# Performance work log

Hardware: AMD Instinct MI355X
Metric: run time of the kernel (lower is better)

## Reference

```python
import jax, jax.numpy as jnp
import numpy as np
from jax import lax

B, T, F, Z, H = 256, 1024, 64, 32, 512


def _lstm_cell(x, h, c, W_ih, W_hh, b_ih, b_hh):
    # gates: [B, 4H], torch LSTMCell gate order i, f, g, o
    g = x @ W_ih.T + b_ih + h @ W_hh.T + b_hh
    i, f, gg, o = jnp.split(g, 4, axis=-1)
    c_new = jax.nn.sigmoid(f) * c + jax.nn.sigmoid(i) * jnp.tanh(gg)
    h_new = jax.nn.sigmoid(o) * jnp.tanh(c_new)
    return h_new, c_new


def setup_inputs() -> dict:
    key = jax.random.key(0)
    ks = jax.random.split(key, 12)
    s = 1.0 / np.sqrt(H)
    return {
        "input": jax.random.normal(ks[0], (B, T, F), dtype=jnp.float32),
        "z": jax.random.normal(ks[1], (B, Z, 1), dtype=jnp.float32),
        "h0": jnp.zeros((B, H), dtype=jnp.float32),
        "c0": jnp.zeros((B, H), dtype=jnp.float32),
        "W_ih1": jax.random.normal(ks[2], (4 * H, F + Z), dtype=jnp.float32) * s,
        "W_hh1": jax.random.normal(ks[3], (4 * H, H), dtype=jnp.float32) * s,
        "b_ih1": jax.random.normal(ks[4], (4 * H,), dtype=jnp.float32) * s,
        "b_hh1": jax.random.normal(ks[5], (4 * H,), dtype=jnp.float32) * s,
        "W_ih2": jax.random.normal(ks[6], (4 * H, H), dtype=jnp.float32) * s,
        "W_hh2": jax.random.normal(ks[7], (4 * H, H), dtype=jnp.float32) * s,
        "b_ih2": jax.random.normal(ks[8], (4 * H,), dtype=jnp.float32) * s,
        "b_hh2": jax.random.normal(ks[9], (4 * H,), dtype=jnp.float32) * s,
        "W_lin": jax.random.normal(ks[10], (1, H), dtype=jnp.float32) * s,
        "b_lin": jax.random.normal(ks[11], (1,), dtype=jnp.float32) * s,
    }


def reference(input, z, h0, c0, W_ih1, W_hh1, b_ih1, b_hh1,
              W_ih2, W_hh2, b_ih2, b_hh2, W_lin, b_lin):
    zf = z[:, :, 0]  # [B, Z], concatenated at every step
    # torch loop iterates i = T-1 ... 0; scan over time-reversed inputs
    xs = jnp.swapaxes(input, 0, 1)[::-1]  # [T, B, F]

    def step(carry, x_t):
        h1, c1, h2, c2 = carry
        xin = jnp.concatenate([x_t, zf], axis=1)  # [B, F+Z]
        h1, c1 = _lstm_cell(xin, h1, c1, W_ih1, W_hh1, b_ih1, b_hh1)
        h2, c2 = _lstm_cell(h1, h2, c2, W_ih2, W_hh2, b_ih2, b_hh2)
        return (h1, c1, h2, c2), h2

    _, ys = lax.scan(step, (h0, c0, h0, c0), xs)
    # outputs[i] = h2 at loop index i; outputs[-1] = outputs[T-1] = first scan step
    last_out = ys[0]
    return last_out @ W_lin.T + b_lin
```

## Files before the change

kernel.cpp:

```cpp
#include <hip/hip_runtime.h>
#include <math.h>

#define NB 256
#define NT 1024
#define NF 64
#define NZ 32
#define NH 512


__device__ __forceinline__ float sigmoidf_(float x) {
    return 1.0f / (1.0f + __expf(-x));
}

__global__ __launch_bounds__(256) void k_prep(
    const float* __restrict__ input, const float* __restrict__ z,
    const float* __restrict__ b_lin, float* __restrict__ xinT,
    float* __restrict__ out)
{
    int idx = blockIdx.x * 256 + threadIdx.x;
    int k  = idx >> 8;
    int bt = idx & 255;
    float v;
    if (k < NF) v = input[(size_t)bt * (NT * NF) + (size_t)(NT - 1) * NF + k];
    else        v = z[bt * NZ + (k - NF)];
    xinT[k * NB + bt] = v;
    if (idx < NB) out[idx] = b_lin[0];
}

__global__ __launch_bounds__(256) void k_lstm1(
    const float* __restrict__ W_ih1, const float* __restrict__ b_ih1,
    const float* __restrict__ b_hh1, const float* __restrict__ xinT,
    float* __restrict__ h1T)
{
    const int lane = threadIdx.x & 63;
    const int wv   = __builtin_amdgcn_readfirstlane(threadIdx.x >> 6);
    const int btb  = blockIdx.x & 3;
    const int jb   = blockIdx.x >> 2;
    const int bt   = btb * 64 + lane;
    const int j0   = jb * 16 + wv * 4;
    const int K    = NF + NZ;

    float acc[4][3];
    #pragma unroll
    for (int jj = 0; jj < 4; ++jj)
        acc[jj][0] = acc[jj][1] = acc[jj][2] = 0.0f;

    const float* __restrict__ wi[4];
    const float* __restrict__ wg[4];
    const float* __restrict__ wo[4];
    #pragma unroll
    for (int jj = 0; jj < 4; ++jj) {
        int j = j0 + jj;
        wi[jj] = W_ih1 + (size_t)j * K;
        wg[jj] = W_ih1 + (size_t)(1024 + j) * K;
        wo[jj] = W_ih1 + (size_t)(1536 + j) * K;
    }

    #pragma unroll 4
    for (int k = 0; k < K; ++k) {
        float h = xinT[k * NB + bt];
        #pragma unroll
        for (int jj = 0; jj < 4; ++jj) {
            acc[jj][0] = fmaf(wi[jj][k], h, acc[jj][0]);
            acc[jj][1] = fmaf(wg[jj][k], h, acc[jj][1]);
            acc[jj][2] = fmaf(wo[jj][k], h, acc[jj][2]);
        }
    }

    #pragma unroll
    for (int jj = 0; jj < 4; ++jj) {
        int j = j0 + jj;
        float gi = acc[jj][0] + b_ih1[j]        + b_hh1[j];
        float gg = acc[jj][1] + b_ih1[1024 + j] + b_hh1[1024 + j];
        float go = acc[jj][2] + b_ih1[1536 + j] + b_hh1[1536 + j];
        float c1 = sigmoidf_(gi) * tanhf(gg);
        float h1 = sigmoidf_(go) * tanhf(c1);
        h1T[j * NB + bt] = h1;
    }
}

__global__ __launch_bounds__(256) void k_lstm2(
    const float* __restrict__ W_ih2, const float* __restrict__ b_ih2,
    const float* __restrict__ b_hh2, const float* __restrict__ W_lin,
    const float* __restrict__ h1T, float* __restrict__ out)
{
    const int lane = threadIdx.x & 63;
    const int wv   = __builtin_amdgcn_readfirstlane(threadIdx.x >> 6);
    const int btb  = blockIdx.x & 3;
    const int jb   = blockIdx.x >> 2;
    const int bt   = btb * 64 + lane;
    const int j0   = jb * 8 + wv * 2;

    float acc[2][3];
    #pragma unroll
    for (int jj = 0; jj < 2; ++jj)
        acc[jj][0] = acc[jj][1] = acc[jj][2] = 0.0f;

    const float* __restrict__ wi[2];
    const float* __restrict__ wg[2];
    const float* __restrict__ wo[2];
    #pragma unroll
    for (int jj = 0; jj < 2; ++jj) {
        int j = j0 + jj;
        wi[jj] = W_ih2 + (size_t)j * NH;
        wg[jj] = W_ih2 + (size_t)(1024 + j) * NH;
        wo[jj] = W_ih2 + (size_t)(1536 + j) * NH;
    }

    #pragma unroll 8
    for (int k = 0; k < NH; ++k) {
        float h = h1T[k * NB + bt];
        #pragma unroll
        for (int jj = 0; jj < 2; ++jj) {
            acc[jj][0] = fmaf(wi[jj][k], h, acc[jj][0]);
            acc[jj][1] = fmaf(wg[jj][k], h, acc[jj][1]);
            acc[jj][2] = fmaf(wo[jj][k], h, acc[jj][2]);
        }
    }

    float partial = 0.0f;
    #pragma unroll
    for (int jj = 0; jj < 2; ++jj) {
        int j = j0 + jj;
        float gi = acc[jj][0] + b_ih2[j]        + b_hh2[j];
        float gg = acc[jj][1] + b_ih2[1024 + j] + b_hh2[1024 + j];
        float go = acc[jj][2] + b_ih2[1536 + j] + b_hh2[1536 + j];
        float c2 = sigmoidf_(gi) * tanhf(gg);
        float h2 = sigmoidf_(go) * tanhf(c2);
        partial  = fmaf(h2, W_lin[j], partial);
    }
    atomicAdd(out + bt, partial);
}

extern "C" void kernel_launch(void* const* d_in, const int* in_sizes, int n_in,
                              void* d_out, int out_size, void* d_ws, size_t ws_size,
                              hipStream_t stream) {
    const float* input = (const float*)d_in[0];
    const float* z     = (const float*)d_in[1];
    const float* W_ih1 = (const float*)d_in[4];
    const float* b_ih1 = (const float*)d_in[6];
    const float* b_hh1 = (const float*)d_in[7];
    const float* W_ih2 = (const float*)d_in[8];
    const float* b_ih2 = (const float*)d_in[10];
    const float* b_hh2 = (const float*)d_in[11];
    const float* W_lin = (const float*)d_in[12];
    const float* b_lin = (const float*)d_in[13];

    float* out  = (float*)d_out;
    float* xinT = (float*)d_ws;
    float* h1T  = xinT + 96 * NB;

    k_prep <<< 96, 256, 0, stream>>>(input, z, b_lin, xinT, out);
    k_lstm1<<<128, 256, 0, stream>>>(W_ih1, b_ih1, b_hh1, xinT, h1T);
    k_lstm2<<<256, 256, 0, stream>>>(W_ih2, b_ih2, b_hh2, W_lin, h1T, out);
}
```

Baseline: 169.2 us.

## Pack activations as float4 along K and split-K reduce second cell across waves

The intermediate activations are stored in a K-interleaved layout so each lane loads a float4 of four consecutive K values, which cuts load instruction count and lets weights be read in groups of four. Layer-1 launches many more small 64-thread blocks with two hidden units each. Layer-2 launches four times as many blocks, splits the K dimension across the four waves and reduces their partial sums through shared memory before the gate math and the atomic output add. This adds more parallelism and fewer loads, at the cost of a block barrier, shared memory traffic and more blocks re-reading the same activations.

```diff
diff --git a/kernel.cpp b/kernel.cpp
--- a/kernel.cpp
+++ b/kernel.cpp
@@ -14,122 +14,131 @@
 
 __global__ __launch_bounds__(256) void k_prep(
     const float* __restrict__ input, const float* __restrict__ z,
-    const float* __restrict__ b_lin, float* __restrict__ xinT,
+    const float* __restrict__ b_lin, float* __restrict__ xin4f,
     float* __restrict__ out)
 {
-    int idx = blockIdx.x * 256 + threadIdx.x;
-    int k  = idx >> 8;
-    int bt = idx & 255;
+    int k  = blockIdx.x;
+    int bt = threadIdx.x;
     float v;
     if (k < NF) v = input[(size_t)bt * (NT * NF) + (size_t)(NT - 1) * NF + k];
     else        v = z[bt * NZ + (k - NF)];
-    xinT[k * NB + bt] = v;
-    if (idx < NB) out[idx] = b_lin[0];
+    xin4f[(k >> 2) * (NB * 4) + bt * 4 + (k & 3)] = v;
+    if (k == 0) out[bt] = b_lin[0];
 }
 
-__global__ __launch_bounds__(256) void k_lstm1(
+__global__ __launch_bounds__(64) void k_lstm1(
     const float* __restrict__ W_ih1, const float* __restrict__ b_ih1,
-    const float* __restrict__ b_hh1, const float* __restrict__ xinT,
-    float* __restrict__ h1T)
+    const float* __restrict__ b_hh1, const float* __restrict__ xin4,
+    float* __restrict__ h1p)
 {
-    const int lane = threadIdx.x & 63;
-    const int wv   = __builtin_amdgcn_readfirstlane(threadIdx.x >> 6);
-    const int btb  = blockIdx.x & 3;
-    const int jb   = blockIdx.x >> 2;
+    const int lane = threadIdx.x;
+    const int btb  = blockIdx.x >> 8;
+    const int g    = blockIdx.x & 255;
     const int bt   = btb * 64 + lane;
-    const int j0   = jb * 16 + wv * 4;
+    const int j0   = 2 * g;
     const int K    = NF + NZ;
 
-    float acc[4][3];
+    const float4* __restrict__ xv = (const float4*)xin4 + bt;
+
+    const float* __restrict__ w[6];
     #pragma unroll
-    for (int jj = 0; jj < 4; ++jj)
-        acc[jj][0] = acc[jj][1] = acc[jj][2] = 0.0f;
-
-    const float* __restrict__ wi[4];
-    const float* __restrict__ wg[4];
-    const float* __restrict__ wo[4];
-    #pragma unroll
-    for (int jj = 0; jj < 4; ++jj) {
-        int j = j0 + jj;
-        wi[jj] = W_ih1 + (size_t)j * K;
-        wg[jj] = W_ih1 + (size_t)(1024 + j) * K;
-        wo[jj] = W_ih1 + (size_t)(1536 + j) * K;
+    for (int u = 0; u < 2; ++u) {
+        w[u * 3 + 0] = W_ih1 + (size_t)(j0 + u) * K;
+        w[u * 3 + 1] = W_ih1 + (size_t)(1024 + j0 + u) * K;
+        w[u * 3 + 2] = W_ih1 + (size_t)(1536 + j0 + u) * K;
     }
 
-    #pragma unroll 4
-    for (int k = 0; k < K; ++k) {
-        float h = xinT[k * NB + bt];
+    float acc[6] = {0, 0, 0, 0, 0, 0};
+    #pragma unroll
+    for (int k4 = 0; k4 < 24; ++k4) {
+        float4 h = xv[k4 * NB];
         #pragma unroll
-        for (int jj = 0; jj < 4; ++jj) {
-            acc[jj][0] = fmaf(wi[jj][k], h, acc[jj][0]);
-            acc[jj][1] = fmaf(wg[jj][k], h, acc[jj][1]);
-            acc[jj][2] = fmaf(wo[jj][k], h, acc[jj][2]);
+        for (int r = 0; r < 6; ++r) {
+            const float* wr = w[r] + k4 * 4;
+            acc[r] = fmaf(wr[0], h.x, acc[r]);
+            acc[r] = fmaf(wr[1], h.y, acc[r]);
+            acc[r] = fmaf(wr[2], h.z, acc[r]);
+            acc[r] = fmaf(wr[3], h.w, acc[r]);
         }
     }
 
+    float hu[2];
     #pragma unroll
-    for (int jj = 0; jj < 4; ++jj) {
-        int j = j0 + jj;
-        float gi = acc[jj][0] + b_ih1[j]        + b_hh1[j];
-        float gg = acc[jj][1] + b_ih1[1024 + j] + b_hh1[1024 + j];
-        float go = acc[jj][2] + b_ih1[1536 + j] + b_hh1[1536 + j];
+    for (int u = 0; u < 2; ++u) {
+        int j = j0 + u;
+        float gi = acc[u * 3 + 0] + b_ih1[j]        + b_hh1[j];
+        float gg = acc[u * 3 + 1] + b_ih1[1024 + j] + b_hh1[1024 + j];
+        float go = acc[u * 3 + 2] + b_ih1[1536 + j] + b_hh1[1536 + j];
         float c1 = sigmoidf_(gi) * tanhf(gg);
-        float h1 = sigmoidf_(go) * tanhf(c1);
-        h1T[j * NB + bt] = h1;
+        hu[u] = sigmoidf_(go) * tanhf(c1);
     }
+    float2 hv = make_float2(hu[0], hu[1]);
+    *(float2*)(h1p + (j0 >> 2) * (NB * 4) + bt * 4 + (j0 & 3)) = hv;
 }
 
 __global__ __launch_bounds__(256) void k_lstm2(
     const float* __restrict__ W_ih2, const float* __restrict__ b_ih2,
     const float* __restrict__ b_hh2, const float* __restrict__ W_lin,
-    const float* __restrict__ h1T, float* __restrict__ out)
+    const float* __restrict__ h1p, float* __restrict__ out)
 {
-    const int lane = threadIdx.x & 63;
-    const int wv   = __builtin_amdgcn_readfirstlane(threadIdx.x >> 6);
-    const int btb  = blockIdx.x & 3;
-    const int jb   = blockIdx.x >> 2;
+    const int tid  = threadIdx.x;
+    const int lane = tid & 63;
+    const int wv   = __builtin_amdgcn_readfirstlane(tid >> 6);
+    const int btb  = blockIdx.x >> 8;
+    const int g    = blockIdx.x & 255;
     const int bt   = btb * 64 + lane;
-    const int j0   = jb * 8 + wv * 2;
+    const int j0   = 2 * g;
 
-    float acc[2][3];
+    const float4* __restrict__ hv = (const float4*)h1p + bt;
+
+    const float* __restrict__ w[6];
     #pragma unroll
-    for (int jj = 0; jj < 2; ++jj)
-        acc[jj][0] = acc[jj][1] = acc[jj][2] = 0.0f;
-
-    const float* __restrict__ wi[2];
-    const float* __restrict__ wg[2];
-    const float* __restrict__ wo[2];
-    #pragma unroll
-    for (int jj = 0; jj < 2; ++jj) {
-        int j = j0 + jj;
-        wi[jj] = W_ih2 + (size_t)j * NH;
-        wg[jj] = W_ih2 + (size_t)(1024 + j) * NH;
-        wo[jj] = W_ih2 + (size_t)(1536 + j) * NH;
+    for (int u = 0; u < 2; ++u) {
+        w[u * 3 + 0] = W_ih2 + (size_t)(j0 + u) * NH;
+        w[u * 3 + 1] = W_ih2 + (size_t)(1024 + j0 + u) * NH;
+        w[u * 3 + 2] = W_ih2 + (size_t)(1536 + j0 + u) * NH;
     }
 
+    float acc[6] = {0, 0, 0, 0, 0, 0};
+    const int k4base = wv * 32;
     #pragma unroll 8
-    for (int k = 0; k < NH; ++k) {
-        float h = h1T[k * NB + bt];
+    for (int k4i = 0; k4i < 32; ++k4i) {
+        int k4 = k4base + k4i;
+        float4 h = hv[k4 * NB];
         #pragma unroll
-        for (int jj = 0; jj < 2; ++jj) {
-            acc[jj][0] = fmaf(wi[jj][k], h, acc[jj][0]);
-            acc[jj][1] = fmaf(wg[jj][k], h, acc[jj][1]);
-            acc[jj][2] = fmaf(wo[jj][k], h, acc[jj][2]);
+        for (int r = 0; r < 6; ++r) {
+            const float* wr = w[r] + k4 * 4;
+            acc[r] = fmaf(wr[0], h.x, acc[r]);
+            acc[r] = fmaf(wr[1], h.y, acc[r]);
+            acc[r] = fmaf(wr[2], h.z, acc[r]);
+            acc[r] = fmaf(wr[3], h.w, acc[r]);
         }
     }
 
-    float partial = 0.0f;
+    __shared__ float red[4][6][64];
     #pragma unroll
-    for (int jj = 0; jj < 2; ++jj) {
-        int j = j0 + jj;
-        float gi = acc[jj][0] + b_ih2[j]        + b_hh2[j];
-        float gg = acc[jj][1] + b_ih2[1024 + j] + b_hh2[1024 + j];
-        float go = acc[jj][2] + b_ih2[1536 + j] + b_hh2[1536 + j];
-        float c2 = sigmoidf_(gi) * tanhf(gg);
-        float h2 = sigmoidf_(go) * tanhf(c2);
-        partial  = fmaf(h2, W_lin[j], partial);
+    for (int r = 0; r < 6; ++r) red[wv][r][lane] = acc[r];
+    __syncthreads();
+
+    if (wv == 0) {
+        float s[6];
+        #pragma unroll
+        for (int r = 0; r < 6; ++r)
+            s[r] = red[0][r][lane] + red[1][r][lane] +
+                   red[2][r][lane] + red[3][r][lane];
+        float partial = 0.0f;
+        #pragma unroll
+        for (int u = 0; u < 2; ++u) {
+            int j = j0 + u;
+            float gi = s[u * 3 + 0] + b_ih2[j]        + b_hh2[j];
+            float gg = s[u * 3 + 1] + b_ih2[1024 + j] + b_hh2[1024 + j];
+            float go = s[u * 3 + 2] + b_ih2[1536 + j] + b_hh2[1536 + j];
+            float c2 = sigmoidf_(gi) * tanhf(gg);
+            float h2 = sigmoidf_(go) * tanhf(c2);
+            partial  = fmaf(h2, W_lin[j], partial);
+        }
+        atomicAdd(out + bt, partial);
     }
-    atomicAdd(out + bt, partial);
 }
 
 extern "C" void kernel_launch(void* const* d_in, const int* in_sizes, int n_in,
@@ -147,10 +156,10 @@
     const float* b_lin = (const float*)d_in[13];
 
     float* out  = (float*)d_out;
-    float* xinT = (float*)d_ws;
-    float* h1T  = xinT + 96 * NB;
+    float* xin4 = (float*)d_ws;
+    float* h1p  = xin4 + 24 * NB * 4;
 
-    k_prep <<< 96, 256, 0, stream>>>(input, z, b_lin, xinT, out);
-    k_lstm1<<<128, 256, 0, stream>>>(W_ih1, b_ih1, b_hh1, xinT, h1T);
-    k_lstm2<<<256, 256, 0, stream>>>(W_ih2, b_ih2, b_hh2, W_lin, h1T, out);
+    k_prep <<<  96, 256, 0, stream>>>(input, z, b_lin, xin4, out);
+    k_lstm1<<<1024,  64, 0, stream>>>(W_ih1, b_ih1, b_hh1, xin4, h1p);
+    k_lstm2<<<1024, 256, 0, stream>>>(W_ih2, b_ih2, b_hh2, W_lin, h1p, out);
 }
```

After: 145.0 us. -14.3%, faster.
